# Performance work log

Hardware: AMD Instinct MI355X
Metric: run time of the kernel (lower is better)

The kernel has to match this reference:

```python
import jax, jax.numpy as jnp
import numpy as np

E = 8          # num_experts
D = 768        # d_model
H = 3072       # d_hidden
TOP_K = 2


def setup_inputs() -> dict:
    key = jax.random.key(0)
    ks = jax.random.split(key, 8)
    s_in = 1.0 / np.sqrt(D)
    s_h = 1.0 / np.sqrt(H)
    return {
        "hidden_states": jax.random.normal(ks[0], (2, 2048, D), dtype=jnp.float32),
        "gate_w": jax.random.normal(ks[1], (E, D), dtype=jnp.float32) * s_in,
        "gate_b": jnp.zeros((E,), dtype=jnp.float32),
        "w1": jax.random.normal(ks[2], (E, H, D), dtype=jnp.float32) * s_in,  # FMoELinear: [E, out, in]
        "b1": jnp.zeros((E, H), dtype=jnp.float32),
        "w2": jax.random.normal(ks[3], (E, D, H), dtype=jnp.float32) * s_h,
        "b2": jnp.zeros((E, D), dtype=jnp.float32),
        "bias": jnp.zeros((D,), dtype=jnp.float32),
    }


def reference(hidden_states, gate_w, gate_b, w1, b1, w2, b2, bias):
    B, S, d = hidden_states.shape
    x = hidden_states.reshape(-1, d)                      # [T, D]
    T = x.shape[0]
    # NaiveGate: linear gate, top-k, softmax over the top-k logits
    logits = x @ gate_w.T + gate_b                        # [T, E]
    top_val, top_idx = jax.lax.top_k(logits, TOP_K)       # [T, K]
    scores = jax.nn.softmax(top_val, axis=-1)             # [T, K]
    # combine weights: [T, E], score mass scattered to chosen experts
    combine = jnp.zeros((T, E), dtype=x.dtype)
    combine = combine.at[jnp.arange(T)[:, None], top_idx].add(scores)
    # expert MLPs (dense over experts, masked combine keeps routing math exact)
    h = jnp.einsum('td,ehd->teh', x, w1) + b1             # [T, E, H]
    h = jax.nn.gelu(h, approximate=False)                 # torch F.gelu (exact erf)
    y = jnp.einsum('teh,edh->ted', h, w2) + b2            # [T, E, D]
    out = jnp.einsum('te,ted->td', combine, y)            # [T, D]
    return out.reshape(B, S, d), bias
```

## Files before the change

### kernel.cpp

```cpp
#include <hip/hip_runtime.h>
#include <hip/hip_bf16.h>

#define DD 768
#define HH 3072
#define NE 8
#define TOPK 2

#define BK 64
#define NB1 (HH / 128)
#define NB2 (DD / 128)
#define SK2 2

typedef __attribute__((ext_vector_type(8))) short short8;
typedef __attribute__((ext_vector_type(4))) float f32x4;

static __device__ __forceinline__ unsigned short f2bf(float v) {
    __hip_bfloat16 b = __float2bfloat16(v);
    return *reinterpret_cast<unsigned short*>(&b);
}

static __device__ __forceinline__ float gelu_f(float v) {
    float s = v * 0.70710678118f;
    float a = fabsf(s);
    float t = __builtin_amdgcn_rcpf(1.f + 0.3275911f * a);
    float poly = t * (0.254829592f + t * (-0.284496736f + t * (1.421413741f +
                 t * (-1.453152027f + t * 1.061405429f))));
    float erfv = 1.f - poly * __expf(-s * s);
    erfv = copysignf(erfv, s);
    return 0.5f * v * (1.f + erfv);
}

__global__ __launch_bounds__(256) void convert_kernel(
    const float* __restrict__ w1, const float* __restrict__ w2,
    unsigned short* __restrict__ w1b, unsigned short* __restrict__ w2b, size_t n)
{
    size_t tid = (size_t)blockIdx.x * blockDim.x + threadIdx.x;
    size_t stride = (size_t)gridDim.x * blockDim.x;
    size_t quarter = n / 4;
    size_t tot = 2 * quarter;
    for (size_t j = tid; j < tot; j += stride) {
        const float* src; unsigned short* dst; size_t off;
        if (j < quarter) { src = w1; dst = w1b; off = j * 4; }
        else             { src = w2; dst = w2b; off = (j - quarter) * 4; }
        float4 v = *reinterpret_cast<const float4*>(&src[off]);
        ushort4 o;
        o.x = f2bf(v.x); o.y = f2bf(v.y); o.z = f2bf(v.z); o.w = f2bf(v.w);
        *reinterpret_cast<ushort4*>(&dst[off]) = o;
    }
}

__global__ __launch_bounds__(256) void init_kernel(int* token_map, int* ctrl, int maxP)
{
    int i = blockIdx.x * blockDim.x + threadIdx.x;
    if (i < maxP) token_map[i] = -1;
    if (i < 64) ctrl[i] = 0;
}

__global__ __launch_bounds__(256) void gate_kernel(
    const float* __restrict__ x, const float* __restrict__ gw, const float* __restrict__ gb,
    int* __restrict__ topk_idx, float* __restrict__ topk_w, int* __restrict__ ctrl, int T)
{
    __shared__ int hist[NE];
    int tid = threadIdx.x;
    if (tid < NE) hist[tid] = 0;
    __syncthreads();

    int w = tid >> 6, lane = tid & 63;
    for (int t = blockIdx.x * 4 + w; t < T; t += gridDim.x * 4) {
        float acc[NE];
#pragma unroll
        for (int e = 0; e < NE; ++e) acc[e] = 0.f;
        const float* xr = x + (size_t)t * DD;
        for (int d = lane; d < DD; d += 64) {
            float xv = xr[d];
#pragma unroll
            for (int e = 0; e < NE; ++e) acc[e] += xv * gw[e * DD + d];
        }
#pragma unroll
        for (int e = 0; e < NE; ++e) {
            float v = acc[e];
            for (int off = 32; off; off >>= 1) v += __shfl_xor(v, off, 64);
            acc[e] = v;
        }
        if (lane == 0) {
            float lg[NE];
#pragma unroll
            for (int e = 0; e < NE; ++e) lg[e] = acc[e] + gb[e];
            int i0 = 0;
#pragma unroll
            for (int e = 1; e < NE; ++e) if (lg[e] > lg[i0]) i0 = e;
            int i1 = -1;
#pragma unroll
            for (int e = 0; e < NE; ++e) {
                if (e == i0) continue;
                if (i1 < 0 || lg[e] > lg[i1]) i1 = e;
            }
            float m = lg[i0];
            float e0 = __expf(lg[i0] - m), e1 = __expf(lg[i1] - m);
            float s = e0 + e1;
            topk_idx[2 * t]     = i0;
            topk_idx[2 * t + 1] = i1;
            topk_w[2 * t]       = e0 / s;
            topk_w[2 * t + 1]   = e1 / s;
            atomicAdd(&hist[i0], 1);
            atomicAdd(&hist[i1], 1);
        }
    }
    __syncthreads();
    if (tid < NE && hist[tid] > 0) atomicAdd(&ctrl[tid], hist[tid]);
}

__global__ void offsets_kernel(int* ctrl)
{
    if (threadIdx.x == 0 && blockIdx.x == 0) {
        int acc = 0, it1 = 0, it2 = 0;
        for (int e = 0; e < NE; ++e) {
            ctrl[16 + e] = acc;
            int nrb = (ctrl[e] + 127) >> 7;
            acc += nrb << 7;
            ctrl[32 + e] = it1; it1 += nrb * NB1;
            ctrl[41 + e] = it2; it2 += nrb * NB2 * SK2;
        }
        ctrl[24] = acc;
        ctrl[40] = it1;
        ctrl[49] = it2;
    }
}

__global__ __launch_bounds__(256) void scatter_kernel(
    const int* __restrict__ topk_idx, const float* __restrict__ topk_w,
    int* ctrl, int* token_map, int* pos_of, float* wpos, int nA)
{
    __shared__ int lh[NE], lbase[NE];
    int tid = threadIdx.x;
    if (tid < NE) lh[tid] = 0;
    __syncthreads();

    int a = blockIdx.x * blockDim.x + tid;
    int e = 0, rank = 0;
    bool valid = (a < nA);
    if (valid) {
        e = topk_idx[a];
        rank = atomicAdd(&lh[e], 1);
    }
    __syncthreads();
    if (tid < NE && lh[tid] > 0)
        lbase[tid] = atomicAdd(&ctrl[8 + tid], lh[tid]);
    __syncthreads();
    if (valid) {
        int p = ctrl[16 + e] + lbase[e] + rank;
        token_map[p] = a;
        pos_of[a] = p;
        wpos[p] = topk_w[a];
    }
}

__global__ __launch_bounds__(256) void gather_kernel(
    const float* __restrict__ x, const int* __restrict__ token_map,
    unsigned short* __restrict__ Xe, int maxP)
{
    int i = blockIdx.x * blockDim.x + threadIdx.x;
    int total = maxP * (DD / 4);
    if (i >= total) return;
    int r = i / (DD / 4);
    int c = (i % (DD / 4)) * 4;
    int a = token_map[r];
    ushort4 o;
    if (a < 0) {
        o.x = o.y = o.z = o.w = 0;
    } else {
        float4 v = *reinterpret_cast<const float4*>(&x[(size_t)(a >> 1) * DD + c]);
        o.x = f2bf(v.x); o.y = f2bf(v.y); o.z = f2bf(v.z); o.w = f2bf(v.w);
    }
    *reinterpret_cast<ushort4*>(&Xe[(size_t)r * DD + c]) = o;
}

static __device__ __forceinline__ void stage_tile(
    const unsigned short* __restrict__ g, int ld, unsigned short* __restrict__ lds)
{
    int tid = threadIdx.x;
#pragma unroll
    for (int r = 0; r < 4; ++r) {
        int j = (r << 8) + tid;
        int row = j >> 3;
        int kc = (j & 7) ^ (row & 7);
        __builtin_amdgcn_global_load_lds(
            (const __attribute__((address_space(1))) void*)(g + (size_t)row * ld + (kc << 3)),
            (__attribute__((address_space(3))) void*)(lds + (j << 3)),
            16, 0, 0);
    }
}

#define LDSF(base, row, kc) \
    reinterpret_cast<const short8*>(&(base)[((((row) << 3) + ((kc) ^ ((row) & 7))) << 3)])

static __device__ __forceinline__ void gemm_item(
    const unsigned short* __restrict__ Abase,
    const unsigned short* __restrict__ Bbase,
    int ld, int nt,
    unsigned short* __restrict__ As, unsigned short* __restrict__ Bs,
    f32x4 acc[4][4], int wr, int wc, int fr, int fq)
{
    const int BUF = 128 * 64;
    stage_tile(Abase, ld, As);
    stage_tile(Bbase, ld, Bs);
    for (int t = 0; t < nt; ++t) {
        int cur = t & 1;
        if (t + 1 < nt) {
            stage_tile(Abase + (size_t)(t + 1) * BK, ld, As + (cur ^ 1) * BUF);
            stage_tile(Bbase + (size_t)(t + 1) * BK, ld, Bs + (cur ^ 1) * BUF);
            asm volatile("s_waitcnt vmcnt(8)" ::: "memory");
        } else {
            asm volatile("s_waitcnt vmcnt(0)" ::: "memory");
        }
        __builtin_amdgcn_s_barrier();
        asm volatile("" ::: "memory");

        const unsigned short* A = As + cur * BUF;
        const unsigned short* B = Bs + cur * BUF;
        short8 a[2][4], b[2][4];
#pragma unroll
        for (int ks = 0; ks < 2; ++ks) {
            int kc = ks * 4 + fq;
#pragma unroll
            for (int m = 0; m < 4; ++m)
                a[ks][m] = *LDSF(A, wr + m * 16 + fr, kc);
#pragma unroll
            for (int n = 0; n < 4; ++n)
                b[ks][n] = *LDSF(B, wc + n * 16 + fr, kc);
        }
        __builtin_amdgcn_s_setprio(1);
#pragma unroll
        for (int ks = 0; ks < 2; ++ks)
#pragma unroll
            for (int m = 0; m < 4; ++m)
#pragma unroll
                for (int n = 0; n < 4; ++n)
                    acc[m][n] = __builtin_amdgcn_mfma_f32_16x16x32_bf16(
                        b[ks][n], a[ks][m], acc[m][n], 0, 0, 0);
        __builtin_amdgcn_s_setprio(0);
        asm volatile("s_waitcnt lgkmcnt(0)" ::: "memory");
        __builtin_amdgcn_s_barrier();
        asm volatile("" ::: "memory");
    }
}


__global__ __launch_bounds__(256, 2) void gemm1_kernel(
    const unsigned short* __restrict__ Xe, const unsigned short* __restrict__ W1b,
    const float* __restrict__ b1, unsigned short* __restrict__ H1,
    int* __restrict__ ctrl)
{
    __shared__ unsigned short As[2 * 128 * 64];
    __shared__ unsigned short Bs[2 * 128 * 64];
    __shared__ int sh_item;
    __shared__ int seg[9], ipfx[9];
    int tid = threadIdx.x;
    if (tid < 9) { seg[tid] = ctrl[16 + tid]; ipfx[tid] = ctrl[32 + tid]; }
    __syncthreads();

    int lane = tid & 63, w = tid >> 6;
    int wr = (w >> 1) * 64, wc = (w & 1) * 64;
    int fr = lane & 15, fq = lane >> 4;
    int tot = ipfx[8];

    for (;;) {
        if (tid == 0) sh_item = atomicAdd(&ctrl[26], 1);
        __syncthreads();
        int item = sh_item;
        if (item >= tot) return;

        int e = 7;
        while (item < ipfx[e]) --e;
        int loc = item - ipfx[e];
        int segbase = seg[e];
        int nrb = (seg[e + 1] - segbase) >> 7;
        int cb = loc / nrb;
        int rb = loc - cb * nrb;
        int rowbase = segbase + (rb << 7);
        int colbase = cb << 7;

        const unsigned short* Abase = Xe + (size_t)rowbase * DD;
        const unsigned short* Bbase = W1b + (size_t)e * HH * DD + (size_t)colbase * DD;

        f32x4 acc[4][4];
#pragma unroll
        for (int m = 0; m < 4; ++m)
#pragma unroll
            for (int n = 0; n < 4; ++n) acc[m][n] = (f32x4){0.f, 0.f, 0.f, 0.f};

        gemm_item(Abase, Bbase, DD, DD / BK, As, Bs, acc, wr, wc, fr, fq);

        float4 bb[4];
#pragma unroll
        for (int n = 0; n < 4; ++n)
            bb[n] = *reinterpret_cast<const float4*>(
                &b1[e * HH + colbase + wc + n * 16 + fq * 4]);
#pragma unroll
        for (int m = 0; m < 4; ++m) {
            int tok = rowbase + wr + m * 16 + fr;
#pragma unroll
            for (int n = 0; n < 4; ++n) {
                int ch = colbase + wc + n * 16 + fq * 4;
                ushort4 o;
                o.x = f2bf(gelu_f(acc[m][n][0] + bb[n].x));
                o.y = f2bf(gelu_f(acc[m][n][1] + bb[n].y));
                o.z = f2bf(gelu_f(acc[m][n][2] + bb[n].z));
                o.w = f2bf(gelu_f(acc[m][n][3] + bb[n].w));
                *reinterpret_cast<ushort4*>(&H1[(size_t)tok * HH + ch]) = o;
            }
        }
    }
}

__global__ __launch_bounds__(256, 2) void gemm2_kernel(
    const unsigned short* __restrict__ H1, const unsigned short* __restrict__ W2b,
    const float* __restrict__ b2, const float* __restrict__ wpos,
    float* __restrict__ Yb, int* __restrict__ ctrl, int maxP)
{
    __shared__ unsigned short As[2 * 128 * 64];
    __shared__ unsigned short Bs[2 * 128 * 64];
    __shared__ int sh_item;
    __shared__ int seg[9], ipfx[9];
    int tid = threadIdx.x;
    if (tid < 9) { seg[tid] = ctrl[16 + tid]; ipfx[tid] = ctrl[41 + tid]; }
    __syncthreads();

    int lane = tid & 63, w = tid >> 6;
    int wr = (w >> 1) * 64, wc = (w & 1) * 64;
    int fr = lane & 15, fq = lane >> 4;
    int tot = ipfx[8];
    size_t Ysz = (size_t)maxP * DD;

    for (;;) {
        if (tid == 0) sh_item = atomicAdd(&ctrl[27], 1);
        __syncthreads();
        int item = sh_item;
        if (item >= tot) return;

        int e = 7;
        while (item < ipfx[e]) --e;
        int loc = item - ipfx[e];
        int segbase = seg[e];
        int nrb = (seg[e + 1] - segbase) >> 7;
        int tmp = loc / nrb;
        int rb = loc - tmp * nrb;
        int sk = tmp & 1;
        int cb = tmp >> 1;
        int rowbase = segbase + (rb << 7);
        int colbase = cb << 7;

        const unsigned short* Abase = H1 + (size_t)rowbase * HH + sk * (HH / 2);
        const unsigned short* Bbase = W2b + (size_t)e * DD * HH + (size_t)colbase * HH + sk * (HH / 2);

        f32x4 acc[4][4];
#pragma unroll
        for (int m = 0; m < 4; ++m)
#pragma unroll
            for (int n = 0; n < 4; ++n) acc[m][n] = (f32x4){0.f, 0.f, 0.f, 0.f};

        gemm_item(Abase, Bbase, HH, HH / BK / SK2, As, Bs, acc, wr, wc, fr, fq);

        float* Yp = Yb + (size_t)sk * Ysz;
        float4 bb[4];
#pragma unroll
        for (int n = 0; n < 4; ++n) {
            float4 b4 = *reinterpret_cast<const float4*>(
                &b2[e * DD + colbase + wc + n * 16 + fq * 4]);
            bb[n].x = 0.5f * b4.x; bb[n].y = 0.5f * b4.y;
            bb[n].z = 0.5f * b4.z; bb[n].w = 0.5f * b4.w;
        }
#pragma unroll
        for (int m = 0; m < 4; ++m) {
            int tok = rowbase + wr + m * 16 + fr;
            float wp = wpos[tok];
#pragma unroll
            for (int n = 0; n < 4; ++n) {
                int ch = colbase + wc + n * 16 + fq * 4;
                float4 o;
                o.x = wp * (acc[m][n][0] + bb[n].x);
                o.y = wp * (acc[m][n][1] + bb[n].y);
                o.z = wp * (acc[m][n][2] + bb[n].z);
                o.w = wp * (acc[m][n][3] + bb[n].w);
                *reinterpret_cast<float4*>(&Yp[(size_t)tok * DD + ch]) = o;
            }
        }
    }
}

__global__ __launch_bounds__(256) void combine_kernel(
    const float* __restrict__ Yb, const int* __restrict__ pos_of,
    const float* __restrict__ bias, float* __restrict__ out, int T, int maxP)
{
    int i = blockIdx.x * blockDim.x + threadIdx.x;
    int total = T * (DD / 4);
    size_t Ysz = (size_t)maxP * DD;
    if (i < total) {
        int t = i / (DD / 4);
        int c = (i % (DD / 4)) * 4;
        int p0 = pos_of[2 * t], p1 = pos_of[2 * t + 1];
        float4 v00 = *reinterpret_cast<const float4*>(&Yb[(size_t)p0 * DD + c]);
        float4 v01 = *reinterpret_cast<const float4*>(&Yb[Ysz + (size_t)p0 * DD + c]);
        float4 v10 = *reinterpret_cast<const float4*>(&Yb[(size_t)p1 * DD + c]);
        float4 v11 = *reinterpret_cast<const float4*>(&Yb[Ysz + (size_t)p1 * DD + c]);
        float4 o;
        o.x = v00.x + v01.x + v10.x + v11.x;
        o.y = v00.y + v01.y + v10.y + v11.y;
        o.z = v00.z + v01.z + v10.z + v11.z;
        o.w = v00.w + v01.w + v10.w + v11.w;
        *reinterpret_cast<float4*>(&out[(size_t)t * DD + c]) = o;
    } else if (i < total + DD / 4) {
        int c = (i - total) * 4;
        *reinterpret_cast<float4*>(&out[(size_t)T * DD + c]) =
            *reinterpret_cast<const float4*>(&bias[c]);
    }
}

extern "C" void kernel_launch(void* const* d_in, const int* in_sizes, int n_in,
                              void* d_out, int out_size, void* d_ws, size_t ws_size,
                              hipStream_t stream)
{
    const float* x    = (const float*)d_in[0];
    const float* gw   = (const float*)d_in[1];
    const float* gb   = (const float*)d_in[2];
    const float* w1   = (const float*)d_in[3];
    const float* b1   = (const float*)d_in[4];
    const float* w2   = (const float*)d_in[5];
    const float* b2   = (const float*)d_in[6];
    const float* bias = (const float*)d_in[7];
    float* out = (float*)d_out;

    int T = in_sizes[0] / DD;
    int nA = T * TOPK;
    int maxP = nA + NE * 128;

    char* ws = (char*)d_ws;
    size_t off = 0;
    auto alloc = [&](size_t bytes) -> char* {
        char* p = ws + off;
        off += (bytes + 255) & ~(size_t)255;
        return p;
    };
    unsigned short* w1b = (unsigned short*)alloc((size_t)NE * HH * DD * 2);
    unsigned short* w2b = (unsigned short*)alloc((size_t)NE * DD * HH * 2);
    unsigned short* Xe  = (unsigned short*)alloc((size_t)maxP * DD * 2);
    unsigned short* H1  = (unsigned short*)alloc((size_t)maxP * HH * 2);
    float*  Yb          = (float*)alloc((size_t)SK2 * maxP * DD * 4);
    int*    topk_idx    = (int*)alloc((size_t)nA * 4);
    float*  topk_w      = (float*)alloc((size_t)nA * 4);
    int*    pos_of      = (int*)alloc((size_t)nA * 4);
    float*  wpos        = (float*)alloc((size_t)maxP * 4);
    int*    token_map   = (int*)alloc((size_t)maxP * 4);
    int*    ctrl        = (int*)alloc(64 * 4);

    size_t nW = (size_t)NE * HH * DD;

    hipLaunchKernelGGL(convert_kernel, dim3(4096), dim3(256), 0, stream,
                       w1, w2, w1b, w2b, nW);
    hipLaunchKernelGGL(init_kernel, dim3((maxP + 255) / 256), dim3(256), 0, stream,
                       token_map, ctrl, maxP);
    hipLaunchKernelGGL(gate_kernel, dim3(512), dim3(256), 0, stream,
                       x, gw, gb, topk_idx, topk_w, ctrl, T);
    hipLaunchKernelGGL(offsets_kernel, dim3(1), dim3(64), 0, stream, ctrl);
    hipLaunchKernelGGL(scatter_kernel, dim3((nA + 255) / 256), dim3(256), 0, stream,
                       topk_idx, topk_w, ctrl, token_map, pos_of, wpos, nA);
    hipLaunchKernelGGL(gather_kernel, dim3((maxP * (DD / 4) + 255) / 256), dim3(256), 0, stream,
                       x, token_map, Xe, maxP);
    hipLaunchKernelGGL(gemm1_kernel, dim3(512), dim3(256), 0, stream,
                       Xe, w1b, b1, H1, ctrl);
    hipLaunchKernelGGL(gemm2_kernel, dim3(512), dim3(256), 0, stream,
                       H1, w2b, b2, wpos, Yb, ctrl, maxP);
    hipLaunchKernelGGL(combine_kernel, dim3((T * (DD / 4) + DD / 4 + 255) / 256, 1, 1), dim3(256), 0, stream,
                       Yb, pos_of, bias, out, T, maxP);
}
```

Measured before the change: 234.6 us.

## Partition GEMM work into per-XCD queues grouped by weight tile for L2 reuse

Replaces the single global atomic work counter in both expert GEMMs with eight queues. Each queue holds the (expert, column-block) pairs with index mod 8, and all row blocks of one pair run back to back. Blocks start at queue blockIdx&7, which on MI355X's round-robin XCD dispatch aims to keep the same weight tiles inside one XCD's L2, and they steal from other queues when their own runs dry. The gate kernel also switches to float4 loads. The cost is extra barriers per item, a linear search over the queue table per item, and reliance on the block-to-XCD mapping.

```diff
diff --git a/kernel.cpp b/kernel.cpp
--- a/kernel.cpp
+++ b/kernel.cpp
@@ -49,11 +49,12 @@
     }
 }
 
-__global__ __launch_bounds__(256) void init_kernel(int* token_map, int* ctrl, int maxP)
+__global__ __launch_bounds__(256) void init_kernel(int* token_map, int* ctrl, int* qcur, int maxP)
 {
     int i = blockIdx.x * blockDim.x + threadIdx.x;
     if (i < maxP) token_map[i] = -1;
     if (i < 64) ctrl[i] = 0;
+    if (i < 256) qcur[i] = 0;
 }
 
 __global__ __launch_bounds__(256) void gate_kernel(
@@ -70,11 +71,14 @@
         float acc[NE];
 #pragma unroll
         for (int e = 0; e < NE; ++e) acc[e] = 0.f;
-        const float* xr = x + (size_t)t * DD;
-        for (int d = lane; d < DD; d += 64) {
-            float xv = xr[d];
-#pragma unroll
-            for (int e = 0; e < NE; ++e) acc[e] += xv * gw[e * DD + d];
+        const float4* xr = reinterpret_cast<const float4*>(x + (size_t)t * DD);
+        for (int d = lane; d < DD / 4; d += 64) {
+            float4 xv = xr[d];
+#pragma unroll
+            for (int e = 0; e < NE; ++e) {
+                float4 gv = *reinterpret_cast<const float4*>(&gw[e * DD + 4 * d]);
+                acc[e] += xv.x * gv.x + xv.y * gv.y + xv.z * gv.z + xv.w * gv.w;
+            }
         }
 #pragma unroll
         for (int e = 0; e < NE; ++e) {
@@ -110,20 +114,37 @@
     if (tid < NE && hist[tid] > 0) atomicAdd(&ctrl[tid], hist[tid]);
 }
 
-__global__ void offsets_kernel(int* ctrl)
+__global__ void offsets_kernel(int* ctrl, int* wq1, int* wq2)
 {
     if (threadIdx.x == 0 && blockIdx.x == 0) {
-        int acc = 0, it1 = 0, it2 = 0;
+        int nrbs[NE];
+        int acc = 0;
         for (int e = 0; e < NE; ++e) {
             ctrl[16 + e] = acc;
             int nrb = (ctrl[e] + 127) >> 7;
+            nrbs[e] = nrb;
             acc += nrb << 7;
-            ctrl[32 + e] = it1; it1 += nrb * NB1;
-            ctrl[41 + e] = it2; it2 += nrb * NB2 * SK2;
         }
         ctrl[24] = acc;
-        ctrl[40] = it1;
-        ctrl[49] = it2;
+        int qc[8], qcum[8];
+        for (int q = 0; q < 8; ++q) { qc[q] = 0; qcum[q] = 0; }
+        for (int pair = 0; pair < NE * NB1; ++pair) {
+            int e = pair / NB1;
+            int q = pair & 7;
+            int s = qc[q]++;
+            qcum[q] += nrbs[e];
+            wq1[(q * 24 + s) * 2 + 0] = pair;
+            wq1[(q * 24 + s) * 2 + 1] = qcum[q];
+        }
+        for (int q = 0; q < 8; ++q) { qc[q] = 0; qcum[q] = 0; }
+        for (int g = 0; g < NE * NB2 * SK2; ++g) {
+            int e = g / (NB2 * SK2);
+            int q = g & 7;
+            int s = qc[q]++;
+            qcum[q] += nrbs[e];
+            wq2[(q * 12 + s) * 2 + 0] = g;
+            wq2[(q * 12 + s) * 2 + 1] = qcum[q];
+        }
     }
 }
 
@@ -249,65 +270,72 @@
 __global__ __launch_bounds__(256, 2) void gemm1_kernel(
     const unsigned short* __restrict__ Xe, const unsigned short* __restrict__ W1b,
     const float* __restrict__ b1, unsigned short* __restrict__ H1,
-    int* __restrict__ ctrl)
+    const int* __restrict__ ctrl, const int* __restrict__ wq1, int* __restrict__ qcur)
 {
     __shared__ unsigned short As[2 * 128 * 64];
     __shared__ unsigned short Bs[2 * 128 * 64];
     __shared__ int sh_item;
-    __shared__ int seg[9], ipfx[9];
+    __shared__ int seg[9];
+    __shared__ int tpair[192], tcum[192];
+
     int tid = threadIdx.x;
-    if (tid < 9) { seg[tid] = ctrl[16 + tid]; ipfx[tid] = ctrl[32 + tid]; }
+    if (tid < 9) seg[tid] = ctrl[16 + tid];
+    if (tid < 192) { tpair[tid] = wq1[2 * tid]; tcum[tid] = wq1[2 * tid + 1]; }
     __syncthreads();
 
     int lane = tid & 63, w = tid >> 6;
     int wr = (w >> 1) * 64, wc = (w & 1) * 64;
     int fr = lane & 15, fq = lane >> 4;
-    int tot = ipfx[8];
-
-    for (;;) {
-        if (tid == 0) sh_item = atomicAdd(&ctrl[26], 1);
-        __syncthreads();
-        int item = sh_item;
-        if (item >= tot) return;
-
-        int e = 7;
-        while (item < ipfx[e]) --e;
-        int loc = item - ipfx[e];
-        int segbase = seg[e];
-        int nrb = (seg[e + 1] - segbase) >> 7;
-        int cb = loc / nrb;
-        int rb = loc - cb * nrb;
-        int rowbase = segbase + (rb << 7);
-        int colbase = cb << 7;
-
-        const unsigned short* Abase = Xe + (size_t)rowbase * DD;
-        const unsigned short* Bbase = W1b + (size_t)e * HH * DD + (size_t)colbase * DD;
-
-        f32x4 acc[4][4];
-#pragma unroll
-        for (int m = 0; m < 4; ++m)
-#pragma unroll
-            for (int n = 0; n < 4; ++n) acc[m][n] = (f32x4){0.f, 0.f, 0.f, 0.f};
-
-        gemm_item(Abase, Bbase, DD, DD / BK, As, Bs, acc, wr, wc, fr, fq);
-
-        float4 bb[4];
-#pragma unroll
-        for (int n = 0; n < 4; ++n)
-            bb[n] = *reinterpret_cast<const float4*>(
-                &b1[e * HH + colbase + wc + n * 16 + fq * 4]);
-#pragma unroll
-        for (int m = 0; m < 4; ++m) {
-            int tok = rowbase + wr + m * 16 + fr;
-#pragma unroll
-            for (int n = 0; n < 4; ++n) {
-                int ch = colbase + wc + n * 16 + fq * 4;
-                ushort4 o;
-                o.x = f2bf(gelu_f(acc[m][n][0] + bb[n].x));
-                o.y = f2bf(gelu_f(acc[m][n][1] + bb[n].y));
-                o.z = f2bf(gelu_f(acc[m][n][2] + bb[n].z));
-                o.w = f2bf(gelu_f(acc[m][n][3] + bb[n].w));
-                *reinterpret_cast<ushort4*>(&H1[(size_t)tok * HH + ch]) = o;
+    int q0 = blockIdx.x & 7;
+
+    for (int off = 0; off < 8; ++off) {
+        int qq = (q0 + off) & 7;
+        int qtot = tcum[qq * 24 + 23];
+        for (;;) {
+            if (tid == 0) sh_item = atomicAdd(&qcur[qq * 16], 1);
+            __syncthreads();
+            int j = sh_item;
+            __syncthreads();
+            if (j >= qtot) break;
+
+            int s = 0;
+            while (tcum[qq * 24 + s] <= j) ++s;
+            int pair = tpair[qq * 24 + s];
+            int start = s ? tcum[qq * 24 + s - 1] : 0;
+            int rb = j - start;
+            int e = pair / NB1, cb = pair - e * NB1;
+            int rowbase = seg[e] + (rb << 7);
+            int colbase = cb << 7;
+
+            const unsigned short* Abase = Xe + (size_t)rowbase * DD;
+            const unsigned short* Bbase = W1b + (size_t)e * HH * DD + (size_t)colbase * DD;
+
+            f32x4 acc[4][4];
+#pragma unroll
+            for (int m = 0; m < 4; ++m)
+#pragma unroll
+                for (int n = 0; n < 4; ++n) acc[m][n] = (f32x4){0.f, 0.f, 0.f, 0.f};
+
+            gemm_item(Abase, Bbase, DD, DD / BK, As, Bs, acc, wr, wc, fr, fq);
+
+            float4 bb[4];
+#pragma unroll
+            for (int n = 0; n < 4; ++n)
+                bb[n] = *reinterpret_cast<const float4*>(
+                    &b1[e * HH + colbase + wc + n * 16 + fq * 4]);
+#pragma unroll
+            for (int m = 0; m < 4; ++m) {
+                int tok = rowbase + wr + m * 16 + fr;
+#pragma unroll
+                for (int n = 0; n < 4; ++n) {
+                    int ch = colbase + wc + n * 16 + fq * 4;
+                    ushort4 o;
+                    o.x = f2bf(gelu_f(acc[m][n][0] + bb[n].x));
+                    o.y = f2bf(gelu_f(acc[m][n][1] + bb[n].y));
+                    o.z = f2bf(gelu_f(acc[m][n][2] + bb[n].z));
+                    o.w = f2bf(gelu_f(acc[m][n][3] + bb[n].w));
+                    *reinterpret_cast<ushort4*>(&H1[(size_t)tok * HH + ch]) = o;
+                }
             }
         }
     }
@@ -316,73 +344,82 @@
 __global__ __launch_bounds__(256, 2) void gemm2_kernel(
     const unsigned short* __restrict__ H1, const unsigned short* __restrict__ W2b,
     const float* __restrict__ b2, const float* __restrict__ wpos,
-    float* __restrict__ Yb, int* __restrict__ ctrl, int maxP)
+    float* __restrict__ Yb, const int* __restrict__ ctrl,
+    const int* __restrict__ wq2, int* __restrict__ qcur, int maxP)
 {
     __shared__ unsigned short As[2 * 128 * 64];
     __shared__ unsigned short Bs[2 * 128 * 64];
     __shared__ int sh_item;
-    __shared__ int seg[9], ipfx[9];
+    __shared__ int seg[9];
+    __shared__ int tpair[96], tcum[96];
+
     int tid = threadIdx.x;
-    if (tid < 9) { seg[tid] = ctrl[16 + tid]; ipfx[tid] = ctrl[41 + tid]; }
+    if (tid < 9) seg[tid] = ctrl[16 + tid];
+    if (tid < 96) { tpair[tid] = wq2[2 * tid]; tcum[tid] = wq2[2 * tid + 1]; }
     __syncthreads();
 
     int lane = tid & 63, w = tid >> 6;
     int wr = (w >> 1) * 64, wc = (w & 1) * 64;
     int fr = lane & 15, fq = lane >> 4;
-    int tot = ipfx[8];
+    int q0 = blockIdx.x & 7;
     size_t Ysz = (size_t)maxP * DD;
 
-    for (;;) {
-        if (tid == 0) sh_item = atomicAdd(&ctrl[27], 1);
-        __syncthreads();
-        int item = sh_item;
-        if (item >= tot) return;
-
-        int e = 7;
-        while (item < ipfx[e]) --e;
-        int loc = item - ipfx[e];
-        int segbase = seg[e];
-        int nrb = (seg[e + 1] - segbase) >> 7;
-        int tmp = loc / nrb;
-        int rb = loc - tmp * nrb;
-        int sk = tmp & 1;
-        int cb = tmp >> 1;
-        int rowbase = segbase + (rb << 7);
-        int colbase = cb << 7;
-
-        const unsigned short* Abase = H1 + (size_t)rowbase * HH + sk * (HH / 2);
-        const unsigned short* Bbase = W2b + (size_t)e * DD * HH + (size_t)colbase * HH + sk * (HH / 2);
-
-        f32x4 acc[4][4];
-#pragma unroll
-        for (int m = 0; m < 4; ++m)
-#pragma unroll
-            for (int n = 0; n < 4; ++n) acc[m][n] = (f32x4){0.f, 0.f, 0.f, 0.f};
-
-        gemm_item(Abase, Bbase, HH, HH / BK / SK2, As, Bs, acc, wr, wc, fr, fq);
-
-        float* Yp = Yb + (size_t)sk * Ysz;
-        float4 bb[4];
-#pragma unroll
-        for (int n = 0; n < 4; ++n) {
-            float4 b4 = *reinterpret_cast<const float4*>(
-                &b2[e * DD + colbase + wc + n * 16 + fq * 4]);
-            bb[n].x = 0.5f * b4.x; bb[n].y = 0.5f * b4.y;
-            bb[n].z = 0.5f * b4.z; bb[n].w = 0.5f * b4.w;
-        }
-#pragma unroll
-        for (int m = 0; m < 4; ++m) {
-            int tok = rowbase + wr + m * 16 + fr;
-            float wp = wpos[tok];
+    for (int off = 0; off < 8; ++off) {
+        int qq = (q0 + off) & 7;
+        int qtot = tcum[qq * 12 + 11];
+        for (;;) {
+            if (tid == 0) sh_item = atomicAdd(&qcur[(8 + qq) * 16], 1);
+            __syncthreads();
+            int j = sh_item;
+            __syncthreads();
+            if (j >= qtot) break;
+
+            int s = 0;
+            while (tcum[qq * 12 + s] <= j) ++s;
+            int g = tpair[qq * 12 + s];
+            int start = s ? tcum[qq * 12 + s - 1] : 0;
+            int rb = j - start;
+            int e = g / (NB2 * SK2);
+            int rem = g - e * (NB2 * SK2);
+            int cb = rem >> 1;
+            int sk = rem & 1;
+            int rowbase = seg[e] + (rb << 7);
+            int colbase = cb << 7;
+
+            const unsigned short* Abase = H1 + (size_t)rowbase * HH + sk * (HH / 2);
+            const unsigned short* Bbase = W2b + (size_t)e * DD * HH + (size_t)colbase * HH + sk * (HH / 2);
+
+            f32x4 acc[4][4];
+#pragma unroll
+            for (int m = 0; m < 4; ++m)
+#pragma unroll
+                for (int n = 0; n < 4; ++n) acc[m][n] = (f32x4){0.f, 0.f, 0.f, 0.f};
+
+            gemm_item(Abase, Bbase, HH, HH / BK / SK2, As, Bs, acc, wr, wc, fr, fq);
+
+            float* Yp = Yb + (size_t)sk * Ysz;
+            float4 bb[4];
 #pragma unroll
             for (int n = 0; n < 4; ++n) {
-                int ch = colbase + wc + n * 16 + fq * 4;
-                float4 o;
-                o.x = wp * (acc[m][n][0] + bb[n].x);
-                o.y = wp * (acc[m][n][1] + bb[n].y);
-                o.z = wp * (acc[m][n][2] + bb[n].z);
-                o.w = wp * (acc[m][n][3] + bb[n].w);
-                *reinterpret_cast<float4*>(&Yp[(size_t)tok * DD + ch]) = o;
+                float4 b4 = *reinterpret_cast<const float4*>(
+                    &b2[e * DD + colbase + wc + n * 16 + fq * 4]);
+                bb[n].x = 0.5f * b4.x; bb[n].y = 0.5f * b4.y;
+                bb[n].z = 0.5f * b4.z; bb[n].w = 0.5f * b4.w;
+            }
+#pragma unroll
+            for (int m = 0; m < 4; ++m) {
+                int tok = rowbase + wr + m * 16 + fr;
+                float wp = wpos[tok];
+#pragma unroll
+                for (int n = 0; n < 4; ++n) {
+                    int ch = colbase + wc + n * 16 + fq * 4;
+                    float4 o;
+                    o.x = wp * (acc[m][n][0] + bb[n].x);
+                    o.y = wp * (acc[m][n][1] + bb[n].y);
+                    o.z = wp * (acc[m][n][2] + bb[n].z);
+                    o.w = wp * (acc[m][n][3] + bb[n].w);
+                    *reinterpret_cast<float4*>(&Yp[(size_t)tok * DD + ch]) = o;
+                }
             }
         }
     }
@@ -452,24 +489,27 @@
     float*  wpos        = (float*)alloc((size_t)maxP * 4);
     int*    token_map   = (int*)alloc((size_t)maxP * 4);
     int*    ctrl        = (int*)alloc(64 * 4);
+    int*    wq1         = (int*)alloc(384 * 4);
+    int*    wq2         = (int*)alloc(192 * 4);
+    int*    qcur        = (int*)alloc(256 * 4);
 
     size_t nW = (size_t)NE * HH * DD;
 
     hipLaunchKernelGGL(convert_kernel, dim3(4096), dim3(256), 0, stream,
                        w1, w2, w1b, w2b, nW);
     hipLaunchKernelGGL(init_kernel, dim3((maxP + 255) / 256), dim3(256), 0, stream,
-                       token_map, ctrl, maxP);
+                       token_map, ctrl, qcur, maxP);
     hipLaunchKernelGGL(gate_kernel, dim3(512), dim3(256), 0, stream,
                        x, gw, gb, topk_idx, topk_w, ctrl, T);
-    hipLaunchKernelGGL(offsets_kernel, dim3(1), dim3(64), 0, stream, ctrl);
+    hipLaunchKernelGGL(offsets_kernel, dim3(1), dim3(64), 0, stream, ctrl, wq1, wq2);
     hipLaunchKernelGGL(scatter_kernel, dim3((nA + 255) / 256), dim3(256), 0, stream,
                        topk_idx, topk_w, ctrl, token_map, pos_of, wpos, nA);
     hipLaunchKernelGGL(gather_kernel, dim3((maxP * (DD / 4) + 255) / 256), dim3(256), 0, stream,
                        x, token_map, Xe, maxP);
     hipLaunchKernelGGL(gemm1_kernel, dim3(512), dim3(256), 0, stream,
-                       Xe, w1b, b1, H1, ctrl);
+                       Xe, w1b, b1, H1, ctrl, wq1, qcur);
     hipLaunchKernelGGL(gemm2_kernel, dim3(512), dim3(256), 0, stream,
-                       H1, w2b, b2, wpos, Yb, ctrl, maxP);
+                       H1, w2b, b2, wpos, Yb, ctrl, wq2, qcur, maxP);
     hipLaunchKernelGGL(combine_kernel, dim3((T * (DD / 4) + DD / 4 + 255) / 256, 1, 1), dim3(256), 0, stream,
                        Yb, pos_of, bias, out, T, maxP);
 }
```

Result: slower. 254.2 us (+8.4%).
